# Optimization experiments

Measured on AMD Instinct MI355X. Metric: run time of the kernel, lower is better.

Reference implementation:

```python
import jax, jax.numpy as jnp
import numpy as np

D = 512
P = 1024
E = 256
OUT = 500


def setup_inputs() -> dict:
    key = jax.random.key(0)
    ks = jax.random.split(key, 10)
    s = 1.0 / np.sqrt(D)
    s2 = 1.0 / np.sqrt(2 * D)
    return {
        "post": jax.random.normal(ks[0], (P, D), dtype=jnp.float32),
        "emoji": jax.random.normal(ks[1], (E, D), dtype=jnp.float32),
        "k1_w": jax.random.normal(ks[2], (D, D), dtype=jnp.float32) * s,
        "k1_b": jax.random.normal(ks[3], (D,), dtype=jnp.float32) * s,
        "k2_w": jax.random.normal(ks[4], (D, D), dtype=jnp.float32) * s,
        "k2_b": jax.random.normal(ks[5], (D,), dtype=jnp.float32) * s,
        "l1_w": jax.random.normal(ks[6], (2 * D, D), dtype=jnp.float32) * s2,
        "l1_b": jax.random.normal(ks[7], (D,), dtype=jnp.float32) * s2,
        "l2_w": jax.random.normal(ks[8], (D, OUT), dtype=jnp.float32) * s,
        "l2_b": jax.random.normal(ks[9], (D if False else OUT,), dtype=jnp.float32) * s,
    }


def reference(post, emoji, k1_w, k1_b, k2_w, k2_b, l1_w, l1_b, l2_w, l2_b):
    # k1/k2 projections: [P, D], [E, D]
    p = post @ k1_w + k1_b
    e = emoji @ k2_w + k2_b
    # l1 on concat([tile(p), tile(e)], -1) == p @ W1_post + e @ W1_emoji + b,
    # broadcast-added over the pairwise grid (same math, avoids explicit tile+cat)
    d = post.shape[1]
    pp = p @ l1_w[:d]   # [P, D]
    ee = e @ l1_w[d:]   # [E, D]
    h = jax.nn.relu(pp[:, None, :] + ee[None, :, :] + l1_b)  # [P, E, D]
    out = jax.nn.relu(h @ l2_w + l2_b)  # [P, E, OUT]
    return out
```

## Files before the change

### kernel.cpp

```cpp
#include <hip/hip_runtime.h>
#include <hip/hip_bf16.h>

#define D_DIM 512
#define P_DIM 1024
#define E_DIM 256
#define OUT_DIM 500

typedef __attribute__((ext_vector_type(8))) __bf16 bf16x8;
typedef __attribute__((ext_vector_type(4))) float f32x4;

__device__ __forceinline__ unsigned short f2bf(float f) {
    unsigned u = __builtin_bit_cast(unsigned, f);
    u += 0x7FFFu + ((u >> 16) & 1u);
    return (unsigned short)(u >> 16);
}

__device__ __forceinline__ unsigned pack2(float a, float b) {
    return (unsigned)f2bf(a) | ((unsigned)f2bf(b) << 16);
}

__global__ void cast_bf16_kernel(const float* __restrict__ in,
                                 unsigned short* __restrict__ out, int n) {
    int i = blockIdx.x * 256 + threadIdx.x;
    if (i < n) out[i] = f2bf(in[i]);
}

__global__ void transpose_cast_kernel(const float* __restrict__ in,
                                      unsigned short* __restrict__ out,
                                      int R, int C, int Cpad) {
    __shared__ float tile[32][33];
    int c0 = blockIdx.x * 32, r0 = blockIdx.y * 32;
    #pragma unroll
    for (int s = 0; s < 32; s += 8) {
        int r = r0 + threadIdx.y + s, c = c0 + threadIdx.x;
        tile[threadIdx.y + s][threadIdx.x] = (r < R && c < C) ? in[r * C + c] : 0.f;
    }
    __syncthreads();
    #pragma unroll
    for (int s = 0; s < 32; s += 8) {
        int c = c0 + threadIdx.y + s, r = r0 + threadIdx.x;
        if (c < Cpad && r < R) out[c * R + r] = f2bf(tile[threadIdx.x][threadIdx.y + s]);
    }
}

__device__ __forceinline__ void store_out(float* p, float v) { *p = v; }
__device__ __forceinline__ void store_out(unsigned short* p, float v) { *p = f2bf(v); }

template <typename OutT>
__global__ __launch_bounds__(256)
void gemm128_kernel(const unsigned short* __restrict__ A,
                    const unsigned short* __restrict__ Bt,
                    const float* __restrict__ bias,
                    OutT* __restrict__ Cd, int M, int N, int K) {
    __shared__ __align__(16) unsigned short As[128 * 40];
    __shared__ __align__(16) unsigned short Bs[128 * 40];
    const int t = threadIdx.x;
    const int m0 = blockIdx.x * 128, n0 = blockIdx.y * 128;
    const int r = t >> 1, kh = (t & 1) * 16;
    const int w = t >> 6, l = t & 63;
    const int wm = (w & 1) * 64, wn = (w >> 1) * 64;
    const int lr = l & 15, lq = l >> 4;

    f32x4 acc[4][4];
    #pragma unroll
    for (int a = 0; a < 4; a++)
        #pragma unroll
        for (int b = 0; b < 4; b++) acc[a][b] = (f32x4){0.f, 0.f, 0.f, 0.f};

    const unsigned short* aRow = &A[(m0 + r) * K];
    const unsigned short* bRow = &Bt[(n0 + r) * K];

    for (int k0 = 0; k0 < K; k0 += 32) {
        uint4 a0 = *reinterpret_cast<const uint4*>(&aRow[k0 + kh]);
        uint4 a1 = *reinterpret_cast<const uint4*>(&aRow[k0 + kh + 8]);
        uint4 b0 = *reinterpret_cast<const uint4*>(&bRow[k0 + kh]);
        uint4 b1 = *reinterpret_cast<const uint4*>(&bRow[k0 + kh + 8]);
        __syncthreads();
        *reinterpret_cast<uint4*>(&As[r * 40 + kh])     = a0;
        *reinterpret_cast<uint4*>(&As[r * 40 + kh + 8]) = a1;
        *reinterpret_cast<uint4*>(&Bs[r * 40 + kh])     = b0;
        *reinterpret_cast<uint4*>(&Bs[r * 40 + kh + 8]) = b1;
        __syncthreads();
        bf16x8 af[4], bfr[4];
        #pragma unroll
        for (int mi = 0; mi < 4; mi++)
            af[mi] = *reinterpret_cast<const bf16x8*>(&As[(wm + mi * 16 + lr) * 40 + lq * 8]);
        #pragma unroll
        for (int ni = 0; ni < 4; ni++)
            bfr[ni] = *reinterpret_cast<const bf16x8*>(&Bs[(wn + ni * 16 + lr) * 40 + lq * 8]);
        #pragma unroll
        for (int mi = 0; mi < 4; mi++)
            #pragma unroll
            for (int ni = 0; ni < 4; ni++)
                acc[mi][ni] = __builtin_amdgcn_mfma_f32_16x16x32_bf16(af[mi], bfr[ni], acc[mi][ni], 0, 0, 0);
    }

    #pragma unroll
    for (int ni = 0; ni < 4; ni++) {
        int n = n0 + wn + ni * 16 + lr;
        float bv = bias ? bias[n] : 0.f;
        #pragma unroll
        for (int mi = 0; mi < 4; mi++) {
            int m = m0 + wm + mi * 16 + lq * 4;
            #pragma unroll
            for (int rg = 0; rg < 4; rg++)
                store_out(&Cd[(m + rg) * N + n], acc[mi][ni][rg] + bv);
        }
    }
}

__global__ __launch_bounds__(512)
void pair_mlp_kernel(const float* __restrict__ pp, const float* __restrict__ ee,
                     const unsigned short* __restrict__ w2t,
                     const float* __restrict__ b2, float* __restrict__ out) {
    __shared__ __align__(16) unsigned short Hs[128 * 520];
    __shared__ __align__(16) unsigned short Bs[256 * 40];

    const int t = threadIdx.x;
    const int mtile = blockIdx.x;
    const int i = mtile >> 1;
    const int j0 = (mtile & 1) * 128;
    const long pairBase = (long)mtile * 128;

    {
        const int rq = t >> 7;
        const int c4 = (t & 127) * 4;
        const f32x4 pv = *reinterpret_cast<const f32x4*>(&pp[i * D_DIM + c4]);
        #pragma unroll 8
        for (int it = 0; it < 32; ++it) {
            int r = it * 4 + rq;
            f32x4 ev = *reinterpret_cast<const f32x4*>(&ee[(j0 + r) * D_DIM + c4]);
            f32x4 s = pv + ev;
            #pragma unroll
            for (int x = 0; x < 4; x++) s[x] = s[x] > 0.f ? s[x] : 0.f;
            unsigned u0, u1;
            asm("v_cvt_pk_bf16_f32 %0, %1, %2" : "=v"(u0) : "v"(s[0]), "v"(s[1]));
            asm("v_cvt_pk_bf16_f32 %0, %1, %2" : "=v"(u1) : "v"(s[2]), "v"(s[3]));
            uint2 hv; hv.x = u0; hv.y = u1;
            *reinterpret_cast<uint2*>(&Hs[r * 520 + c4]) = hv;
        }
    }

    const int r = t >> 1, kh = (t & 1) * 16;
    const int w = t >> 6, l = t & 63;
    const int wm = (w & 1) * 64, wn = (w >> 1) * 64;
    const int lr = l & 15, lq = l >> 4;

    f32x4 acc[4][4];
    #pragma unroll
    for (int a = 0; a < 4; a++)
        #pragma unroll
        for (int b = 0; b < 4; b++) acc[a][b] = (f32x4){0.f, 0.f, 0.f, 0.f};

    const unsigned short* wRow = &w2t[r * D_DIM + kh];

    uint4 c0 = *reinterpret_cast<const uint4*>(wRow);
    uint4 c1 = *reinterpret_cast<const uint4*>(wRow + 8);
    __syncthreads();
    *reinterpret_cast<uint4*>(&Bs[r * 40 + kh])     = c0;
    *reinterpret_cast<uint4*>(&Bs[r * 40 + kh + 8]) = c1;
    __syncthreads();

    for (int u = 0; u < 32; ++u) {
        const int k0 = (u & 15) * 32;

        uint4 n0v, n1v;
        if (u < 31) {
            const int un = u + 1;
            const unsigned short* p = wRow + ((un >> 4) * 256) * D_DIM + (un & 15) * 32;
            n0v = *reinterpret_cast<const uint4*>(p);
            n1v = *reinterpret_cast<const uint4*>(p + 8);
        }

        bf16x8 af[4], bfr[4];
        #pragma unroll
        for (int mi = 0; mi < 4; mi++)
            af[mi] = *reinterpret_cast<const bf16x8*>(&Hs[(wm + mi * 16 + lr) * 520 + k0 + lq * 8]);
        #pragma unroll
        for (int ni = 0; ni < 4; ni++)
            bfr[ni] = *reinterpret_cast<const bf16x8*>(&Bs[(wn + ni * 16 + lr) * 40 + lq * 8]);
        #pragma unroll
        for (int mi = 0; mi < 4; mi++)
            #pragma unroll
            for (int ni = 0; ni < 4; ni++)
                acc[mi][ni] = __builtin_amdgcn_mfma_f32_16x16x32_bf16(af[mi], bfr[ni], acc[mi][ni], 0, 0, 0);

        __syncthreads();
        if (u < 31) {
            *reinterpret_cast<uint4*>(&Bs[r * 40 + kh])     = n0v;
            *reinterpret_cast<uint4*>(&Bs[r * 40 + kh + 8]) = n1v;
        }

        if ((u & 15) == 15) {
            const int nbase = (u >> 4) * 256;
            #pragma unroll
            for (int ni = 0; ni < 4; ni++) {
                int n = nbase + wn + ni * 16 + lr;
                if (n < OUT_DIM) {
                    float bv = b2[n];
                    #pragma unroll
                    for (int mi = 0; mi < 4; mi++) {
                        long m = pairBase + wm + mi * 16 + lq * 4;
                        float* op = &out[m * OUT_DIM + n];
                        #pragma unroll
                        for (int rg = 0; rg < 4; rg++) {
                            float v = acc[mi][ni][rg] + bv;
                            op[(long)rg * OUT_DIM] = v > 0.f ? v : 0.f;
                        }
                    }
                }
                #pragma unroll
                for (int mi = 0; mi < 4; mi++) acc[mi][ni] = (f32x4){0.f, 0.f, 0.f, 0.f};
            }
        }
        __syncthreads();
    }
}

extern "C" void kernel_launch(void* const* d_in, const int* in_sizes, int n_in,
                              void* d_out, int out_size, void* d_ws, size_t ws_size,
                              hipStream_t stream) {
    const float* post  = (const float*)d_in[0];
    const float* emoji = (const float*)d_in[1];
    const float* k1_w  = (const float*)d_in[2];
    const float* k1_b  = (const float*)d_in[3];
    const float* k2_w  = (const float*)d_in[4];
    const float* k2_b  = (const float*)d_in[5];
    const float* l1_w  = (const float*)d_in[6];
    const float* l1_b  = (const float*)d_in[7];
    const float* l2_w  = (const float*)d_in[8];
    const float* l2_b  = (const float*)d_in[9];
    float* out = (float*)d_out;

    char* wp = (char*)d_ws;
    auto alloc = [&](size_t bytes) { char* q = wp; wp += (bytes + 255) & ~(size_t)255; return q; };
    unsigned short* post_bf  = (unsigned short*)alloc(P_DIM * D_DIM * 2);
    unsigned short* emoji_bf = (unsigned short*)alloc(E_DIM * D_DIM * 2);
    unsigned short* k1_wt    = (unsigned short*)alloc(D_DIM * D_DIM * 2);
    unsigned short* k2_wt    = (unsigned short*)alloc(D_DIM * D_DIM * 2);
    unsigned short* l1at     = (unsigned short*)alloc(D_DIM * D_DIM * 2);
    unsigned short* l1bt     = (unsigned short*)alloc(D_DIM * D_DIM * 2);
    unsigned short* w2t      = (unsigned short*)alloc(512 * 512 * 2);
    unsigned short* p_bf     = (unsigned short*)alloc(P_DIM * D_DIM * 2);
    unsigned short* e_bf     = (unsigned short*)alloc(E_DIM * D_DIM * 2);
    float* pp  = (float*)alloc(P_DIM * D_DIM * 4);
    float* eeb = (float*)alloc(E_DIM * D_DIM * 4);

    cast_bf16_kernel<<<P_DIM * D_DIM / 256, 256, 0, stream>>>(post, post_bf, P_DIM * D_DIM);
    cast_bf16_kernel<<<E_DIM * D_DIM / 256, 256, 0, stream>>>(emoji, emoji_bf, E_DIM * D_DIM);

    dim3 tb(32, 8);
    transpose_cast_kernel<<<dim3(16, 16), tb, 0, stream>>>(k1_w, k1_wt, 512, 512, 512);
    transpose_cast_kernel<<<dim3(16, 16), tb, 0, stream>>>(k2_w, k2_wt, 512, 512, 512);
    transpose_cast_kernel<<<dim3(16, 16), tb, 0, stream>>>(l1_w, l1at, 512, 512, 512);
    transpose_cast_kernel<<<dim3(16, 16), tb, 0, stream>>>(l1_w + 512 * 512, l1bt, 512, 512, 512);
    transpose_cast_kernel<<<dim3(16, 16), tb, 0, stream>>>(l2_w, w2t, 512, 500, 512);

    gemm128_kernel<unsigned short><<<dim3(8, 4), 256, 0, stream>>>(post_bf, k1_wt, k1_b, p_bf, 1024, 512, 512);
    gemm128_kernel<unsigned short><<<dim3(2, 4), 256, 0, stream>>>(emoji_bf, k2_wt, k2_b, e_bf, 256, 512, 512);
    gemm128_kernel<float><<<dim3(8, 4), 256, 0, stream>>>(p_bf, l1at, (const float*)nullptr, pp, 1024, 512, 512);
    gemm128_kernel<float><<<dim3(2, 4), 256, 0, stream>>>(e_bf, l1bt, l1_b, eeb, 256, 512, 512);

    pair_mlp_kernel<<<dim3(2048), 512, 0, stream>>>(pp, eeb, w2t, l2_b, out);
}
```

Baseline: 946.6 us.

## Load W2 fragments directly from global and compute both output halves in one pass

The pair MLP kernel drops the shared-memory staging buffer for W2 and its per-step barriers. Each wave now reads its B fragments straight from global or L2 memory and holds accumulators for both 256-wide output halves, so the K loop runs once instead of twice. It also adds a min-2-blocks launch bound. The trade-off is doubled accumulator registers (128 floats) under a tighter register cap, which could cause spills, plus uncoalesced global fragment loads with no prefetch.

```diff
diff --git a/kernel.cpp b/kernel.cpp
--- a/kernel.cpp
+++ b/kernel.cpp
@@ -13,10 +13,6 @@
     unsigned u = __builtin_bit_cast(unsigned, f);
     u += 0x7FFFu + ((u >> 16) & 1u);
     return (unsigned short)(u >> 16);
-}
-
-__device__ __forceinline__ unsigned pack2(float a, float b) {
-    return (unsigned)f2bf(a) | ((unsigned)f2bf(b) << 16);
 }
 
 __global__ void cast_bf16_kernel(const float* __restrict__ in,
@@ -109,12 +105,11 @@
     }
 }
 
-__global__ __launch_bounds__(512)
+__global__ __launch_bounds__(512, 2)
 void pair_mlp_kernel(const float* __restrict__ pp, const float* __restrict__ ee,
                      const unsigned short* __restrict__ w2t,
                      const float* __restrict__ b2, float* __restrict__ out) {
     __shared__ __align__(16) unsigned short Hs[128 * 520];
-    __shared__ __align__(16) unsigned short Bs[256 * 40];
 
     const int t = threadIdx.x;
     const int mtile = blockIdx.x;
@@ -140,80 +135,55 @@
             *reinterpret_cast<uint2*>(&Hs[r * 520 + c4]) = hv;
         }
     }
-
-    const int r = t >> 1, kh = (t & 1) * 16;
+    __syncthreads();
+
     const int w = t >> 6, l = t & 63;
-    const int wm = (w & 1) * 64, wn = (w >> 1) * 64;
+    const int wm = (w & 1) * 64;
+    const int wn = (w >> 1) * 64;
     const int lr = l & 15, lq = l >> 4;
 
-    f32x4 acc[4][4];
+    f32x4 acc[4][8];
     #pragma unroll
     for (int a = 0; a < 4; a++)
         #pragma unroll
-        for (int b = 0; b < 4; b++) acc[a][b] = (f32x4){0.f, 0.f, 0.f, 0.f};
-
-    const unsigned short* wRow = &w2t[r * D_DIM + kh];
-
-    uint4 c0 = *reinterpret_cast<const uint4*>(wRow);
-    uint4 c1 = *reinterpret_cast<const uint4*>(wRow + 8);
-    __syncthreads();
-    *reinterpret_cast<uint4*>(&Bs[r * 40 + kh])     = c0;
-    *reinterpret_cast<uint4*>(&Bs[r * 40 + kh + 8]) = c1;
-    __syncthreads();
-
-    for (int u = 0; u < 32; ++u) {
-        const int k0 = (u & 15) * 32;
-
-        uint4 n0v, n1v;
-        if (u < 31) {
-            const int un = u + 1;
-            const unsigned short* p = wRow + ((un >> 4) * 256) * D_DIM + (un & 15) * 32;
-            n0v = *reinterpret_cast<const uint4*>(p);
-            n1v = *reinterpret_cast<const uint4*>(p + 8);
-        }
-
-        bf16x8 af[4], bfr[4];
+        for (int b = 0; b < 8; b++) acc[a][b] = (f32x4){0.f, 0.f, 0.f, 0.f};
+
+    const unsigned short* wBase = &w2t[(wn + lr) * D_DIM + lq * 8];
+
+    for (int k0 = 0; k0 < D_DIM; k0 += 32) {
+        bf16x8 af[4];
         #pragma unroll
         for (int mi = 0; mi < 4; mi++)
             af[mi] = *reinterpret_cast<const bf16x8*>(&Hs[(wm + mi * 16 + lr) * 520 + k0 + lq * 8]);
-        #pragma unroll
-        for (int ni = 0; ni < 4; ni++)
-            bfr[ni] = *reinterpret_cast<const bf16x8*>(&Bs[(wn + ni * 16 + lr) * 40 + lq * 8]);
-        #pragma unroll
-        for (int mi = 0; mi < 4; mi++)
-            #pragma unroll
-            for (int ni = 0; ni < 4; ni++)
+        bf16x8 bfr[8];
+        #pragma unroll
+        for (int ni = 0; ni < 8; ni++) {
+            const int rowOff = (((ni >> 2) * 256) + (ni & 3) * 16) * D_DIM;
+            bfr[ni] = *reinterpret_cast<const bf16x8*>(&wBase[rowOff + k0]);
+        }
+        #pragma unroll
+        for (int mi = 0; mi < 4; mi++)
+            #pragma unroll
+            for (int ni = 0; ni < 8; ni++)
                 acc[mi][ni] = __builtin_amdgcn_mfma_f32_16x16x32_bf16(af[mi], bfr[ni], acc[mi][ni], 0, 0, 0);
-
-        __syncthreads();
-        if (u < 31) {
-            *reinterpret_cast<uint4*>(&Bs[r * 40 + kh])     = n0v;
-            *reinterpret_cast<uint4*>(&Bs[r * 40 + kh + 8]) = n1v;
-        }
-
-        if ((u & 15) == 15) {
-            const int nbase = (u >> 4) * 256;
-            #pragma unroll
-            for (int ni = 0; ni < 4; ni++) {
-                int n = nbase + wn + ni * 16 + lr;
-                if (n < OUT_DIM) {
-                    float bv = b2[n];
-                    #pragma unroll
-                    for (int mi = 0; mi < 4; mi++) {
-                        long m = pairBase + wm + mi * 16 + lq * 4;
-                        float* op = &out[m * OUT_DIM + n];
-                        #pragma unroll
-                        for (int rg = 0; rg < 4; rg++) {
-                            float v = acc[mi][ni][rg] + bv;
-                            op[(long)rg * OUT_DIM] = v > 0.f ? v : 0.f;
-                        }
-                    }
+    }
+
+    #pragma unroll
+    for (int ni = 0; ni < 8; ni++) {
+        int n = (ni >> 2) * 256 + wn + (ni & 3) * 16 + lr;
+        if (n < OUT_DIM) {
+            float bv = b2[n];
+            #pragma unroll
+            for (int mi = 0; mi < 4; mi++) {
+                long m = pairBase + wm + mi * 16 + lq * 4;
+                float* op = &out[m * OUT_DIM + n];
+                #pragma unroll
+                for (int rg = 0; rg < 4; rg++) {
+                    float v = acc[mi][ni][rg] + bv;
+                    op[(long)rg * OUT_DIM] = v > 0.f ? v : 0.f;
                 }
-                #pragma unroll
-                for (int mi = 0; mi < 4; mi++) acc[mi][ni] = (f32x4){0.f, 0.f, 0.f, 0.f};
             }
         }
-        __syncthreads();
     }
 }
 
```

After: 978.8 us. 3.4% more time.
